# Kernel tuning notes

Hardware: AMD Instinct MI355X
Metric: run time of the kernel (lower is better)

The kernel has to match this reference:

```python
import jax, jax.numpy as jnp
import numpy as np

N_QUBITS = 4
N_LAYERS = 2

# wire 0 is the most-significant bit of the flattened [2,2,2,2] state (PennyLane default.qubit order)
_bits = ((np.arange(16)[:, None] >> np.array([3, 2, 1, 0])) & 1)
ZMAT = jnp.asarray(1.0 - 2.0 * _bits, dtype=np.float32)  # [16, 4]; column q = PauliZ eigenvalue on wire q
IDX = jnp.asarray(np.indices((2, 2, 2, 2)))  # [4,2,2,2,2] bit grids for building diagonal gates


def _apply_1q(state, mat, wire):
    # state: [N,2,2,2,2] complex64, mat: [2,2] complex64 acting on `wire`
    s = jnp.moveaxis(state, 1 + wire, -1)
    s = s @ mat.T
    return jnp.moveaxis(s, -1, 1 + wire)


def _simulate(angles, weights):
    # angles: [N,4] per-patch RY angles; weights: [N_LAYERS, 2*N_QUBITS]
    # H then RY(theta) on |0> per qubit -> product state; build it as an outer product.
    c = jnp.cos(angles * 0.5)
    s = jnp.sin(angles * 0.5)
    inv_sqrt2 = jnp.float32(2.0 ** -0.5)
    qvecs = jnp.stack([(c - s) * inv_sqrt2, (c + s) * inv_sqrt2], axis=-1)  # [N,4,2]
    state = jnp.einsum('na,nb,nc,nd->nabcd', qvecs[:, 0], qvecs[:, 1], qvecs[:, 2], qvecs[:, 3])
    state = state.astype(jnp.complex64)
    for layer in range(N_LAYERS):
        # CRZ(phi) = diag(1,1,e^{-i phi/2},e^{+i phi/2}); all 4 CRZs of a layer fuse into one diagonal
        D = jnp.ones((2, 2, 2, 2), jnp.complex64)
        for i in range(N_QUBITS):
            phi = weights[layer, i]
            f = jnp.stack([jnp.ones(2, jnp.complex64),
                           jnp.exp(1j * phi * jnp.array([-0.5, 0.5], jnp.float32))])  # [control, target]
            D = D * f[IDX[i], IDX[(i + 1) % N_QUBITS]]
        state = state * D[None]
        for q in range(N_QUBITS):
            t = weights[layer, N_QUBITS + q] * 0.5
            ct, st = jnp.cos(t), jnp.sin(t)
            mat = jnp.stack([jnp.stack([ct, -st]), jnp.stack([st, ct])]).astype(jnp.complex64)
            state = _apply_1q(state, mat, q)
    probs = jnp.abs(state.reshape(state.shape[0], 16)) ** 2
    return probs @ ZMAT  # [N,4] expval(PauliZ_q)


def _quanv_forward(x, weights):
    B, C, H, W = x.shape  # C == 1 so each 2x2 patch flattens to exactly 4 angles
    P = (H // 2) * (W // 2)
    patches = x.reshape(B, H // 2, 2, W // 2, 2)
    patches = jnp.transpose(patches, (0, 1, 3, 2, 4)).reshape(B * P, 4)  # row-major (i,j), (di,dj) flatten
    out = _simulate(patches, weights)  # [B*P, 4]
    # torch loop appends [B,4] per patch then cats on dim 1 -> patch-major layout
    return out.reshape(B, P * 4)


def setup_inputs():
    key = jax.random.key(0)
    k1, k2 = jax.random.split(key)
    x = jax.random.uniform(k1, (256, 1, 128, 128), dtype=jnp.float32) * jnp.pi
    weights = jax.random.uniform(k2, (2, 8), dtype=jnp.float32) * (2.0 * jnp.pi)
    return {"x": x, "weights": weights}


def reference(x, weights):
    return _quanv_forward(x, weights)
```

## Files before the change

kernel.cpp:

```cpp
#include <hip/hip_runtime.h>


static __device__ __forceinline__ int bit_of(int m, int q) { return (m >> (3 - q)) & 1; }

__global__ __launch_bounds__(256) void quanv_setup(const float* __restrict__ w,
                                                   float* __restrict__ Dout) {
    __shared__ float Ur[16][16], Ui[16][16];
    __shared__ float Cs[324], Ts[324];
    const int tid = threadIdx.x;
    for (int i0 = tid; i0 < 324; i0 += 256) Cs[i0] = 0.f;

    if (tid < 16) {
        float sr[16], si[16];
        for (int m = 0; m < 16; ++m) { sr[m] = (m == tid) ? 1.f : 0.f; si[m] = 0.f; }
        for (int layer = 0; layer < 2; ++layer) {
            float phi[4], ry[4];
            for (int q = 0; q < 4; ++q) { phi[q] = w[layer * 8 + q]; ry[q] = w[layer * 8 + 4 + q]; }
            for (int m = 0; m < 16; ++m) {
                float th = 0.f;
                for (int q = 0; q < 4; ++q)
                    if (bit_of(m, q)) th += phi[q] * (bit_of(m, (q + 1) & 3) ? 0.5f : -0.5f);
                float cs = cosf(th), sn = sinf(th);
                float r  = sr[m] * cs - si[m] * sn;
                float ii = sr[m] * sn + si[m] * cs;
                sr[m] = r; si[m] = ii;
            }
            for (int q = 0; q < 4; ++q) {
                float t = ry[q] * 0.5f;
                float ct = cosf(t), st = sinf(t);
                int stride = 8 >> q;
                for (int m = 0; m < 16; ++m) {
                    if (m & stride) continue;
                    int m1 = m + stride;
                    float r0 = sr[m], r1 = sr[m1];
                    float i0 = si[m], i1 = si[m1];
                    sr[m]  = ct * r0 - st * r1;  sr[m1] = st * r0 + ct * r1;
                    si[m]  = ct * i0 - st * i1;  si[m1] = st * i0 + ct * i1;
                }
            }
        }
        for (int m = 0; m < 16; ++m) { Ur[m][tid] = sr[m]; Ui[m][tid] = si[m]; }
    }
    __syncthreads();

    {
        const int j = tid >> 4, k = tid & 15;
        float a0 = 0.f, a1 = 0.f, a2 = 0.f, a3 = 0.f;
        for (int m = 0; m < 16; ++m) {
            float s = Ur[m][j] * Ur[m][k] + Ui[m][j] * Ui[m][k];
            a0 += bit_of(m, 0) ? -s : s;
            a1 += bit_of(m, 1) ? -s : s;
            a2 += bit_of(m, 2) ? -s : s;
            a3 += bit_of(m, 3) ? -s : s;
        }
        int bin = 0;
        for (int q = 0; q < 4; ++q) bin = bin * 3 + bit_of(j, q) + bit_of(k, q);
        atomicAdd(&Cs[bin * 4 + 0], a0);
        atomicAdd(&Cs[bin * 4 + 1], a1);
        atomicAdd(&Cs[bin * 4 + 2], a2);
        atomicAdd(&Cs[bin * 4 + 3], a3);
    }
    __syncthreads();

#pragma unroll
    for (int j = 0; j < 4; ++j) {
        const int pv = (j == 0) ? 27 : (j == 1) ? 9 : (j == 2) ? 3 : 1;
        const float* src = (j & 1) ? Ts : Cs;
        float*       dst = (j & 1) ? Cs : Ts;
        for (int e = tid; e < 324; e += 256) {
            int bin = e >> 2, qo = e & 3;
            int d = (bin / pv) % 3;
            int base = bin - d * pv;
            float i0 = src[(base         ) * 4 + qo];
            float i1 = src[(base +     pv) * 4 + qo];
            float i2 = src[(base + 2 * pv) * 4 + qo];
            dst[e] = (d == 0) ? 0.5f * (i0 + i2)
                   : (d == 1) ? 0.5f * (i2 - i0)
                              : 0.5f * i1;
        }
        __syncthreads();
    }
    for (int i0 = tid; i0 < 324; i0 += 256) Dout[i0] = Cs[i0];
}

__global__ __launch_bounds__(256) void quanv_main(const float2* __restrict__ x2,
                                                  const float* __restrict__ D,
                                                  float4* __restrict__ out) {
    const int tid = blockIdx.x * 256 + threadIdx.x;
    const int b = tid >> 12;
    const int p = tid & 4095;
    const int pi = p >> 6, pj = p & 63;
    const float2* row = x2 + (size_t)b * 8192 + (size_t)(2 * pi) * 64 + pj;
    float2 a01 = row[0];
    float2 a23 = row[64];

    float s0, c0, s1, c1, s2, c2, s3, c3;
    __sincosf(a01.x, &s0, &c0);
    __sincosf(a01.y, &s1, &c1);
    __sincosf(a23.x, &s2, &c2);
    __sincosf(a23.y, &s3, &c3);

    float P01[9], P23[9];
    P01[1] = s1;      P01[2] = c1;      P01[3] = s0;      P01[6] = c0;
    P01[4] = s0 * s1; P01[5] = s0 * c1; P01[7] = c0 * s1; P01[8] = c0 * c1;
    P23[1] = s3;      P23[2] = c3;      P23[3] = s2;      P23[6] = c2;
    P23[4] = s2 * s3; P23[5] = s2 * c3; P23[7] = c2 * s3; P23[8] = c2 * c3;

    float o0, o1, o2, o3;
#pragma unroll
    for (int b01 = 0; b01 < 9; ++b01) {
        const float* Db = D + b01 * 36;
        float g0 = Db[0], g1 = Db[1], g2 = Db[2], g3 = Db[3];
#pragma unroll
        for (int b23 = 1; b23 < 9; ++b23) {
            float pq = P23[b23];
            g0 = fmaf(Db[b23 * 4 + 0], pq, g0);
            g1 = fmaf(Db[b23 * 4 + 1], pq, g1);
            g2 = fmaf(Db[b23 * 4 + 2], pq, g2);
            g3 = fmaf(Db[b23 * 4 + 3], pq, g3);
        }
        if (b01 == 0) { o0 = g0; o1 = g1; o2 = g2; o3 = g3; }
        else {
            float pp = P01[b01];
            o0 = fmaf(g0, pp, o0); o1 = fmaf(g1, pp, o1);
            o2 = fmaf(g2, pp, o2); o3 = fmaf(g3, pp, o3);
        }
    }
    out[tid] = make_float4(o0, o1, o2, o3);
}

extern "C" void kernel_launch(void* const* d_in, const int* in_sizes, int n_in,
                              void* d_out, int out_size, void* d_ws, size_t ws_size,
                              hipStream_t stream) {
    const float* x = (const float*)d_in[0];
    const float* w = (const float*)d_in[1];
    float* Dt = (float*)d_ws;
    float4* outv = (float4*)d_out;

    quanv_setup<<<1, 256, 0, stream>>>(w, Dt);

    const int n_patches = in_sizes[0] / 4;
    quanv_main<<<n_patches / 256, 256, 0, stream>>>((const float2*)x, Dt, outv);
}
```

Baseline: 87.42 us.

## Parallelize unitary construction across all threads with wavefront shuffles

```diff
diff --git a/kernel.cpp b/kernel.cpp
--- a/kernel.cpp
+++ b/kernel.cpp
@@ -7,39 +7,45 @@
                                                    float* __restrict__ Dout) {
     __shared__ float Ur[16][16], Ui[16][16];
     __shared__ float Cs[324], Ts[324];
+    __shared__ float crz_c[2][16], crz_s[2][16];
+    __shared__ float ry_c[2][4], ry_s[2][4];
     const int tid = threadIdx.x;
     for (int i0 = tid; i0 < 324; i0 += 256) Cs[i0] = 0.f;
 
-    if (tid < 16) {
-        float sr[16], si[16];
-        for (int m = 0; m < 16; ++m) { sr[m] = (m == tid) ? 1.f : 0.f; si[m] = 0.f; }
+    if (tid < 32) {
+        const int layer = tid >> 4, m = tid & 15;
+        float th = 0.f;
+        for (int q = 0; q < 4; ++q)
+            if (bit_of(m, q)) th += w[layer * 8 + q] * (bit_of(m, (q + 1) & 3) ? 0.5f : -0.5f);
+        sincosf(th, &crz_s[layer][m], &crz_c[layer][m]);
+    } else if (tid < 40) {
+        const int layer = (tid - 32) >> 2, q = tid & 3;
+        sincosf(w[layer * 8 + 4 + q] * 0.5f, &ry_s[layer][q], &ry_c[layer][q]);
+    }
+    __syncthreads();
+
+    {
+        const int j = tid >> 4, m = tid & 15;
+        float ar = (m == j) ? 1.f : 0.f, ai = 0.f;
+#pragma unroll
         for (int layer = 0; layer < 2; ++layer) {
-            float phi[4], ry[4];
-            for (int q = 0; q < 4; ++q) { phi[q] = w[layer * 8 + q]; ry[q] = w[layer * 8 + 4 + q]; }
-            for (int m = 0; m < 16; ++m) {
-                float th = 0.f;
-                for (int q = 0; q < 4; ++q)
-                    if (bit_of(m, q)) th += phi[q] * (bit_of(m, (q + 1) & 3) ? 0.5f : -0.5f);
-                float cs = cosf(th), sn = sinf(th);
-                float r  = sr[m] * cs - si[m] * sn;
-                float ii = sr[m] * sn + si[m] * cs;
-                sr[m] = r; si[m] = ii;
-            }
+            const float cs = crz_c[layer][m], sn = crz_s[layer][m];
+            const float r = ar * cs - ai * sn;
+            ai = ar * sn + ai * cs;
+            ar = r;
+#pragma unroll
             for (int q = 0; q < 4; ++q) {
-                float t = ry[q] * 0.5f;
-                float ct = cosf(t), st = sinf(t);
-                int stride = 8 >> q;
-                for (int m = 0; m < 16; ++m) {
-                    if (m & stride) continue;
-                    int m1 = m + stride;
-                    float r0 = sr[m], r1 = sr[m1];
-                    float i0 = si[m], i1 = si[m1];
-                    sr[m]  = ct * r0 - st * r1;  sr[m1] = st * r0 + ct * r1;
-                    si[m]  = ct * i0 - st * i1;  si[m1] = st * i0 + ct * i1;
-                }
+                const int stride = 8 >> q;
+                const float ct = ry_c[layer][q], st = ry_s[layer][q];
+                const float sgn = (m & stride) ? st : -st;
+                const float pr = __shfl_xor(ar, stride, 64);
+                const float pi_ = __shfl_xor(ai, stride, 64);
+                ar = fmaf(sgn, pr, ct * ar);
+                ai = fmaf(sgn, pi_, ct * ai);
             }
         }
-        for (int m = 0; m < 16; ++m) { Ur[m][tid] = sr[m]; Ui[m][tid] = si[m]; }
+        Ur[m][j] = ar;
+        Ui[m][j] = ai;
     }
     __syncthreads();
 
```

Result: faster. 79.33 us (-9.3%).
